# Performance work log

Hardware: AMD Instinct MI355X
Metric: run time of the kernel (lower is better)

The kernel has to match this reference:

```python
import jax, jax.numpy as jnp
import numpy as np

N = 100000          # nodes
E = 1600000         # edges (avg degree 16)
NUM_NODES = 100000  # embedding vocab
EMB = 128
HID = 64
G = 256             # graphs in the batch


def setup_inputs() -> dict:
    key = jax.random.key(0)
    ks = jax.random.split(key, 14)
    x_ids = jax.random.randint(ks[0], (N,), 0, NUM_NODES)
    edge_index = jax.random.randint(ks[1], (2, E), 0, N)
    batch = jnp.sort(jax.random.randint(ks[2], (N,), 0, G))
    s = 0.05
    emb = jax.random.normal(ks[3], (NUM_NODES, EMB), jnp.float32) * s
    W1 = jax.random.normal(ks[4], (EMB, HID), jnp.float32) * s
    b1 = jnp.zeros((HID,), jnp.float32)
    W2 = jax.random.normal(ks[5], (HID, HID), jnp.float32) * s
    b2 = jnp.zeros((HID,), jnp.float32)
    W3 = jax.random.normal(ks[6], (HID, HID), jnp.float32) * s
    b3 = jnp.zeros((HID,), jnp.float32)
    Wf1 = jax.random.normal(ks[7], (HID, HID), jnp.float32) * s
    bf1 = jnp.zeros((HID,), jnp.float32)
    Wf2 = jax.random.normal(ks[8], (HID, 1), jnp.float32) * s
    bf2 = jnp.zeros((1,), jnp.float32)
    return dict(x_ids=x_ids, edge_index=edge_index, batch=batch, emb=emb,
                W1=W1, b1=b1, W2=W2, b2=b2, W3=W3, b3=b3,
                Wf1=Wf1, bf1=bf1, Wf2=Wf2, bf2=bf2)


def gcn_conv(x, W, b, src, dst, num_nodes):
    # PyG GCNConv: x' = D^{-1/2} (A + I) D^{-1/2} (x W) + b
    xw = x @ W  # [N, out]
    ones = jnp.ones(src.shape[0], x.dtype)
    deg = jax.ops.segment_sum(ones, dst, num_segments=num_nodes) + 1.0  # self-loop
    dinv = jax.lax.rsqrt(deg)
    coef = dinv[src] * dinv[dst]  # per-edge norm
    agg = jax.ops.segment_sum(xw[src] * coef[:, None], dst, num_segments=num_nodes)
    agg = agg + xw * (dinv * dinv)[:, None]  # self-loop message
    return agg + b


def reference(x_ids, edge_index, batch, emb, W1, b1, W2, b2, W3, b3, Wf1, bf1, Wf2, bf2):
    src, dst = edge_index[0], edge_index[1]
    x = emb[x_ids]                                   # [N, EMB]
    x = jax.nn.relu(gcn_conv(x, W1, b1, src, dst, N))
    x = jax.nn.relu(gcn_conv(x, W2, b2, src, dst, N))
    x = jax.nn.relu(gcn_conv(x, W3, b3, src, dst, N))
    # global mean pool per graph
    counts = jax.ops.segment_sum(jnp.ones(N, x.dtype), batch, num_segments=G)
    pooled = jax.ops.segment_sum(x, batch, num_segments=G) / jnp.maximum(counts, 1.0)[:, None]
    h = jax.nn.relu(pooled @ Wf1 + bf1)
    out = (h @ Wf2 + bf2).squeeze(-1)                # [G]
    return jax.nn.sigmoid(out)
```

## Files before the change

kernel.cpp:

```cpp
#include <hip/hip_runtime.h>
#include <hip/hip_bf16.h>
#include <hip/hip_fp8.h>


typedef unsigned char u8;
typedef unsigned short u16;
typedef unsigned int u32;

#define FSCALE 256.0f
#define DINV_SCALE 0.0625f

__device__ __forceinline__ float fp8d(u32 b) {
#if __has_builtin(__builtin_amdgcn_cvt_f32_fp8)
  return __builtin_amdgcn_cvt_f32_fp8((int)b, 0);
#else
  __hip_fp8_e4m3 t; t.__x = (__hip_fp8_storage_t)b; return (float)t;
#endif
}
__device__ __forceinline__ u32 fp8e1(float f) {
#if __has_builtin(__builtin_amdgcn_cvt_pk_fp8_f32)
  return (u32)__builtin_amdgcn_cvt_pk_fp8_f32(f, 0.f, 0, false) & 0xffu;
#else
  __hip_fp8_e4m3 t(f); return (u32)t.__x;
#endif
}
__device__ __forceinline__ u32 fp8e4(float f0, float f1, float f2, float f3) {
#if __has_builtin(__builtin_amdgcn_cvt_pk_fp8_f32)
  int r = 0;
  r = __builtin_amdgcn_cvt_pk_fp8_f32(f0, f1, r, false);
  r = __builtin_amdgcn_cvt_pk_fp8_f32(f2, f3, r, true);
  return (u32)r;
#else
  __hip_fp8_e4m3 a(f0), b(f1), c(f2), d(f3);
  return (u32)a.__x | ((u32)b.__x << 8) | ((u32)c.__x << 16) | ((u32)d.__x << 24);
#endif
}

__global__ __launch_bounds__(256) void k_init(int* __restrict__ cnt8, int n8,
                                              u8* __restrict__ rowA, u8* __restrict__ rowB) {
  int i = blockIdx.x * blockDim.x + threadIdx.x;
  int stride = gridDim.x * blockDim.x;
  for (; i < n8; i += stride) cnt8[i] = 0;
  if (blockIdx.x == 0 && threadIdx.x < 64) {
    rowA[threadIdx.x] = 0;
    rowB[threadIdx.x] = 0;
  }
}

__global__ __launch_bounds__(256) void k_count_rank(const int* __restrict__ dst, int* __restrict__ cnt8,
                                                    int* __restrict__ rank, int e_count, int n) {
  int e = blockIdx.x * blockDim.x + threadIdx.x;
  if (e < e_count) {
    int p = blockIdx.x & 7;
    rank[e] = atomicAdd(&cnt8[p * n + dst[e]], 1);
  }
}

__global__ __launch_bounds__(256) void k_scan1(const int* __restrict__ cnt8, int n, int* __restrict__ bsum) {
  __shared__ int s[256];
  int b = blockIdx.x, t = threadIdx.x;
  int base = b * 1024;
  int sum = 0;
  #pragma unroll
  for (int i = 0; i < 4; ++i) {
    int idx = base + t + i * 256;
    if (idx < n) {
      int c = 0;
      #pragma unroll
      for (int q = 0; q < 8; ++q) c += cnt8[q * n + idx];
      sum += (c + 7) & ~7;
    }
  }
  s[t] = sum; __syncthreads();
  for (int off = 128; off > 0; off >>= 1) {
    if (t < off) s[t] += s[t + off];
    __syncthreads();
  }
  if (t == 0) bsum[b] = s[0];
}

__global__ __launch_bounds__(128) void k_scan2(int* __restrict__ bsum, int nb, int* __restrict__ total_out) {
  __shared__ int sh[128];
  int t = threadIdx.x;
  sh[t] = (t < nb) ? bsum[t] : 0;
  __syncthreads();
  for (int off = 1; off < 128; off <<= 1) {
    int x = sh[t];
    int y = (t >= off) ? sh[t - off] : 0;
    __syncthreads();
    sh[t] = x + y;
    __syncthreads();
  }
  if (t < nb) bsum[t] = (t == 0) ? 0 : sh[t - 1];
  if (t == 0) *total_out = sh[127];
}

__global__ __launch_bounds__(256) void k_scan3(int* __restrict__ cnt8, int n,
                                               const int* __restrict__ bsum_ex, int* __restrict__ offsets,
                                               float* __restrict__ dinv, u32* __restrict__ csr) {
  __shared__ int sh[256];
  int b = blockIdx.x, t = threadIdx.x;
  int base = b * 1024 + t * 4;
  int cq[4][8];
  int c[4], v[4];
  #pragma unroll
  for (int i = 0; i < 4; ++i) {
    c[i] = 0;
    #pragma unroll
    for (int q = 0; q < 8; ++q) {
      int x = (base + i < n) ? cnt8[q * n + base + i] : 0;
      cq[i][q] = x;
      c[i] += x;
    }
    v[i] = (c[i] + 7) & ~7;
    if (base + i < n) dinv[base + i] = rsqrtf((float)c[i] + 1.0f) * DINV_SCALE;
  }
  sh[t] = v[0] + v[1] + v[2] + v[3];
  __syncthreads();
  for (int off = 1; off < 256; off <<= 1) {
    int x = sh[t];
    int y = (t >= off) ? sh[t - off] : 0;
    __syncthreads();
    sh[t] = x + y;
    __syncthreads();
  }
  int run = bsum_ex[b] + ((t == 0) ? 0 : sh[t - 1]);
  #pragma unroll
  for (int i = 0; i < 4; ++i) {
    if (base + i < n) {
      offsets[base + i] = run;
      int pb = run;
      #pragma unroll
      for (int q = 0; q < 8; ++q) {
        cnt8[q * n + base + i] = pb;
        pb += cq[i][q];
      }
      for (int j = run + c[i]; j < run + v[i]; ++j) csr[j] = (u32)n;
      run += v[i];
    }
  }
  if (b == 0 && t == 0) dinv[n] = 0.f;
}

__global__ __launch_bounds__(256, 4) void k_mm1_scatter(
    const int* __restrict__ ids, const float* __restrict__ emb,
    const float* __restrict__ W1, u8* __restrict__ out, int n, int mmb,
    const int* __restrict__ src, const int* __restrict__ dst,
    const int* __restrict__ rank, const int* __restrict__ pbase,
    u32* __restrict__ csr, int e_count) {
  if ((int)blockIdx.x >= mmb) {
    int eb = blockIdx.x - mmb;
    int e = eb * 256 + threadIdx.x;
    if (e < e_count) {
      int p = eb & 7;
      int d = dst[e];
      int pos = pbase[p * n + d] + rank[e];
      __builtin_nontemporal_store((u32)src[e], &csr[pos]);
    }
    return;
  }

  const int lane = threadIdx.x & 63;
  const int w = threadIdx.x >> 6;
  const int r = blockIdx.x * 256 + w * 64 + lane;
  const int rid = ids[(r < n) ? r : (n - 1)];
  const float4* __restrict__ xrow = reinterpret_cast<const float4*>(emb + (size_t)rid * 128);

  float acc[64];
  #pragma unroll
  for (int j = 0; j < 64; ++j) acc[j] = 0.f;

  #pragma unroll 1
  for (int s = 0; s < 4; ++s) {
    float4 xb[8];
    #pragma unroll
    for (int i = 0; i < 8; ++i) xb[i] = xrow[s * 8 + i];
    const float* __restrict__ wbase = W1 + (size_t)(s * 32) * 64;
    #pragma unroll
    for (int i = 0; i < 8; ++i) {
      const float* __restrict__ w0 = wbase + (i * 4) * 64;
      #pragma unroll
      for (int j = 0; j < 64; ++j) {
        acc[j] = fmaf(xb[i].x, w0[j], acc[j]);
        acc[j] = fmaf(xb[i].y, w0[64 + j], acc[j]);
        acc[j] = fmaf(xb[i].z, w0[128 + j], acc[j]);
        acc[j] = fmaf(xb[i].w, w0[192 + j], acc[j]);
      }
    }
  }

  if (r < n) {
    u8* op = out + (size_t)r * 64;
    #pragma unroll
    for (int q = 0; q < 4; ++q) {
      uint4 pk;
      pk.x = fp8e4(acc[q * 16 + 0] * FSCALE, acc[q * 16 + 1] * FSCALE,
                   acc[q * 16 + 2] * FSCALE, acc[q * 16 + 3] * FSCALE);
      pk.y = fp8e4(acc[q * 16 + 4] * FSCALE, acc[q * 16 + 5] * FSCALE,
                   acc[q * 16 + 6] * FSCALE, acc[q * 16 + 7] * FSCALE);
      pk.z = fp8e4(acc[q * 16 + 8] * FSCALE, acc[q * 16 + 9] * FSCALE,
                   acc[q * 16 + 10] * FSCALE, acc[q * 16 + 11] * FSCALE);
      pk.w = fp8e4(acc[q * 16 + 12] * FSCALE, acc[q * 16 + 13] * FSCALE,
                   acc[q * 16 + 14] * FSCALE, acc[q * 16 + 15] * FSCALE);
      *reinterpret_cast<uint4*>(op + q * 16) = pk;
    }
  }
}


template <bool FINAL>
__global__ __launch_bounds__(256) void k_agg(const u8* __restrict__ xw, const u32* __restrict__ csr,
                                             const int* __restrict__ offs, const float* __restrict__ dinv,
                                             const float* __restrict__ bias, const float* __restrict__ Wn,
                                             u8* __restrict__ out, int n) {
  const int lane = threadIdx.x & 63;
  const int w = threadIdx.x >> 6;
  const float bl = bias[lane];
  const int ngroups = (n + 3) >> 2;
  const int nwaves = gridDim.x * 4;

  for (int grp = blockIdx.x * 4 + w; grp < ngroups; grp += nwaves) {
    const int v0 = grp * 4;
    const int c1 = (v0 + 1 < n) ? v0 + 1 : n;
    const int c2 = (v0 + 2 < n) ? v0 + 2 : n;
    const int c3 = (v0 + 3 < n) ? v0 + 3 : n;
    const int b0 = offs[v0], b1 = offs[c1], b2 = offs[c2], b3 = offs[c3];
    const int b4 = offs[(v0 + 4 < n) ? v0 + 4 : n];

    const float d0 = dinv[v0];
    const float d1 = dinv[(c1 < n) ? c1 : v0];
    const float d2 = dinv[(c2 < n) ? c2 : v0];
    const float d3 = dinv[(c3 < n) ? c3 : v0];
    float acc0 = fmaf(fp8d(xw[(size_t)v0 * 64 + lane]) * d0, d0, bl);
    float acc1 = (c1 < n) ? fmaf(fp8d(xw[(size_t)c1 * 64 + lane]) * d1, d1, bl) : 0.f;
    float acc2 = (c2 < n) ? fmaf(fp8d(xw[(size_t)c2 * 64 + lane]) * d2, d2, bl) : 0.f;
    float acc3 = (c3 < n) ? fmaf(fp8d(xw[(size_t)c3 * 64 + lane]) * d3, d3, bl) : 0.f;

    int e = b0;
    while (e < b4) {
      int cc = b4 - e;
      cc = (cc < 64) ? cc : 64;
      u32 ce = (u32)n;
      if (lane < cc) ce = csr[e + lane];
      for (int bs = 0; bs < cc; bs += 8) {
        float xv[8], dv[8];
        #pragma unroll
        for (int t = 0; t < 8; ++t) {
          int sb = __builtin_amdgcn_readlane((int)ce, bs + t);
          xv[t] = fp8d(xw[(size_t)sb * 64 + lane]);
          dv[t] = dinv[sb];
        }
        float tmp = 0.f;
        #pragma unroll
        for (int t = 0; t < 8; ++t) tmp = fmaf(xv[t], dv[t], tmp);
        const int ep = e + bs;
        if (ep < b1) acc0 = fmaf(tmp, d0, acc0);
        else if (ep < b2) acc1 = fmaf(tmp, d1, acc1);
        else if (ep < b3) acc2 = fmaf(tmp, d2, acc2);
        else acc3 = fmaf(tmp, d3, acc3);
      }
      e += cc;
    }

    float h0 = fmaxf(acc0, 0.f), h1 = fmaxf(acc1, 0.f);
    float h2 = fmaxf(acc2, 0.f), h3 = fmaxf(acc3, 0.f);
    if constexpr (FINAL) {
      out[(size_t)v0 * 64 + lane] = (u8)fp8e1(h0 * FSCALE);
      if (c1 < n) out[(size_t)c1 * 64 + lane] = (u8)fp8e1(h1 * FSCALE);
      if (c2 < n) out[(size_t)c2 * 64 + lane] = (u8)fp8e1(h2 * FSCALE);
      if (c3 < n) out[(size_t)c3 * 64 + lane] = (u8)fp8e1(h3 * FSCALE);
    } else {
      const int hb0 = __float_as_int(h0), hb1 = __float_as_int(h1);
      const int hb2 = __float_as_int(h2), hb3 = __float_as_int(h3);
      float o0 = 0.f, o1 = 0.f, o2 = 0.f, o3 = 0.f;
      #pragma unroll
      for (int k = 0; k < 64; ++k) {
        float wk = Wn[k * 64 + lane];
        o0 = fmaf(__int_as_float(__builtin_amdgcn_readlane(hb0, k)), wk, o0);
        o1 = fmaf(__int_as_float(__builtin_amdgcn_readlane(hb1, k)), wk, o1);
        o2 = fmaf(__int_as_float(__builtin_amdgcn_readlane(hb2, k)), wk, o2);
        o3 = fmaf(__int_as_float(__builtin_amdgcn_readlane(hb3, k)), wk, o3);
      }
      out[(size_t)v0 * 64 + lane] = (u8)fp8e1(o0 * FSCALE);
      if (c1 < n) out[(size_t)c1 * 64 + lane] = (u8)fp8e1(o1 * FSCALE);
      if (c2 < n) out[(size_t)c2 * 64 + lane] = (u8)fp8e1(o2 * FSCALE);
      if (c3 < n) out[(size_t)c3 * 64 + lane] = (u8)fp8e1(o3 * FSCALE);
    }
  }
}

__global__ __launch_bounds__(256) void k_pool(const u8* __restrict__ x, const int* __restrict__ batch, int n,
                                              const float* __restrict__ Wf1, const float* __restrict__ bf1,
                                              const float* __restrict__ Wf2, const float* __restrict__ bf2,
                                              float* __restrict__ out) {
  int g = blockIdx.x;
  int tid = threadIdx.x, lane = tid & 63, w = tid >> 6;
  int a = 0, b = n;
  while (a < b) { int m = (a + b) >> 1; if (batch[m] < g) a = m + 1; else b = m; }
  int lo = a;
  b = n;
  while (a < b) { int m = (a + b) >> 1; if (batch[m] < g + 1) a = m + 1; else b = m; }
  int hi = a;

  float acc = 0.f;
  for (int r = lo + w; r < hi; r += 4) acc += fp8d(x[(size_t)r * 64 + lane]);
  __shared__ float red[4][64];
  __shared__ float mean[64];
  red[w][lane] = acc;
  __syncthreads();
  if (w == 0) {
    float s = red[0][lane] + red[1][lane] + red[2][lane] + red[3][lane];
    mean[lane] = s / (fmaxf((float)(hi - lo), 1.0f) * FSCALE);
  }
  __syncthreads();
  if (w == 0) {
    float h = bf1[lane];
    #pragma unroll
    for (int k = 0; k < 64; ++k) h = fmaf(mean[k], Wf1[k * 64 + lane], h);
    h = fmaxf(h, 0.f);
    float vv = h * Wf2[lane];
    for (int off = 32; off > 0; off >>= 1) vv += __shfl_down(vv, off, 64);
    if (lane == 0) out[g] = 1.0f / (1.0f + expf(-(vv + bf2[0])));
  }
}

static inline char* align256(char* p) {
  return (char*)(((uintptr_t)p + 255) & ~(uintptr_t)255);
}

extern "C" void kernel_launch(void* const* d_in, const int* in_sizes, int n_in,
                              void* d_out, int out_size, void* d_ws, size_t ws_size,
                              hipStream_t stream) {
  const int*   x_ids = (const int*)d_in[0];
  const int*   edge  = (const int*)d_in[1];
  const int*   batch = (const int*)d_in[2];
  const float* emb   = (const float*)d_in[3];
  const float* W1    = (const float*)d_in[4];
  const float* b1    = (const float*)d_in[5];
  const float* W2    = (const float*)d_in[6];
  const float* b2    = (const float*)d_in[7];
  const float* W3    = (const float*)d_in[8];
  const float* b3    = (const float*)d_in[9];
  const float* Wf1   = (const float*)d_in[10];
  const float* bf1   = (const float*)d_in[11];
  const float* Wf2   = (const float*)d_in[12];
  const float* bf2   = (const float*)d_in[13];
  float* out = (float*)d_out;

  const int N = in_sizes[0];
  const int E = in_sizes[1] / 2;
  const int G = out_size;
  const int* e_src = edge;
  const int* e_dst = edge + E;

  const size_t EPAD = (size_t)E + 8 * (size_t)(N + 1) + 64;

  char* p = (char*)d_ws;
  u8*    bufA = (u8*)p;               p = align256(p + (size_t)(N + 1) * 64);
  u8*    bufB = (u8*)p;               p = align256(p + (size_t)(N + 1) * 64);
  u32*   csr  = (u32*)p;              p = align256(p + EPAD * 4);
  int*   rank = (int*)p;              p = align256(p + (size_t)E * 4);
  float* dinv = (float*)p;            p = align256(p + (size_t)(N + 1) * 4);
  int*   cnt8 = (int*)p;              p = align256(p + (size_t)8 * N * 4);
  int*   offs = (int*)p;              p = align256(p + (size_t)(N + 1) * 4);
  int*   bsum = (int*)p;              p = align256(p + (size_t)1024 * 4);
  (void)ws_size; (void)n_in;

  const int nb_scan = (N + 1023) / 1024;
  dim3 blk(256);

  k_init<<<dim3(512), blk, 0, stream>>>(cnt8, 8 * N, bufA + (size_t)N * 64, bufB + (size_t)N * 64);
  k_count_rank<<<dim3((E + 255) / 256), blk, 0, stream>>>(e_dst, cnt8, rank, E, N);
  k_scan1<<<dim3(nb_scan), blk, 0, stream>>>(cnt8, N, bsum);
  k_scan2<<<dim3(1), dim3(128), 0, stream>>>(bsum, nb_scan, offs + N);
  k_scan3<<<dim3(nb_scan), blk, 0, stream>>>(cnt8, N, bsum, offs, dinv, csr);

  const int mmb = (N + 255) / 256;
  const int scb = (E + 255) / 256;
  k_mm1_scatter<<<dim3(mmb + scb), blk, 0, stream>>>(
      x_ids, emb, W1, bufA, N, mmb,
      e_src, e_dst, rank, cnt8, csr, E);

  k_agg<false><<<dim3(2048), blk, 0, stream>>>(bufA, csr, offs, dinv, b1, W2, bufB, N);
  k_agg<false><<<dim3(2048), blk, 0, stream>>>(bufB, csr, offs, dinv, b2, W3, bufA, N);
  k_agg<true><<<dim3(2048), blk, 0, stream>>>(bufA, csr, offs, dinv, b3, nullptr, bufB, N);

  k_pool<<<dim3(G), blk, 0, stream>>>(bufB, batch, N, Wf1, bf1, Wf2, bf2, out);
}
```

Baseline: 397.9 us.

## Pre-scale node features by source dinv and pipeline fixed 64-edge gathers

Stored fp8 node features are now pre-multiplied by their own inverse-sqrt degree. This happens in the first matmul epilogue and in each aggregation's output, so the edge loop no longer gathers dinv[src] per edge and just sums decoded values. The inner loop now always processes a full 64-edge chunk with two 8-register gather buffers interleaved with compute, to overlap loads and arithmetic. Out-of-range lanes read the zero padding row, and the CSR pad grows to cover over-reads. The fixed chunk size wastes gathers on short tails, and folding dinv into the stored values changes the fp8 quantization range.

```diff
diff --git a/kernel.cpp b/kernel.cpp
--- a/kernel.cpp
+++ b/kernel.cpp
@@ -8,7 +8,8 @@
 typedef unsigned int u32;
 
 #define FSCALE 256.0f
-#define DINV_SCALE 0.0625f
+#define SINV (1.0f / 256.0f)
+#define S2 65536.0f
 
 __device__ __forceinline__ float fp8d(u32 b) {
 #if __has_builtin(__builtin_amdgcn_cvt_f32_fp8)
@@ -97,7 +98,7 @@
 
 __global__ __launch_bounds__(256) void k_scan3(int* __restrict__ cnt8, int n,
                                                const int* __restrict__ bsum_ex, int* __restrict__ offsets,
-                                               float* __restrict__ dinv, u32* __restrict__ csr) {
+                                               float* __restrict__ dsc, u32* __restrict__ csr) {
   __shared__ int sh[256];
   int b = blockIdx.x, t = threadIdx.x;
   int base = b * 1024 + t * 4;
@@ -113,7 +114,7 @@
       c[i] += x;
     }
     v[i] = (c[i] + 7) & ~7;
-    if (base + i < n) dinv[base + i] = rsqrtf((float)c[i] + 1.0f) * DINV_SCALE;
+    if (base + i < n) dsc[base + i] = rsqrtf((float)c[i] + 1.0f) * SINV;
   }
   sh[t] = v[0] + v[1] + v[2] + v[3];
   __syncthreads();
@@ -139,7 +140,7 @@
       run += v[i];
     }
   }
-  if (b == 0 && t == 0) dinv[n] = 0.f;
+  if (b == 0 && t == 0) dsc[n] = 0.f;
 }
 
 __global__ __launch_bounds__(256, 4) void k_mm1_scatter(
@@ -147,7 +148,7 @@
     const float* __restrict__ W1, u8* __restrict__ out, int n, int mmb,
     const int* __restrict__ src, const int* __restrict__ dst,
     const int* __restrict__ rank, const int* __restrict__ pbase,
-    u32* __restrict__ csr, int e_count) {
+    const float* __restrict__ dsc, u32* __restrict__ csr, int e_count) {
   if ((int)blockIdx.x >= mmb) {
     int eb = blockIdx.x - mmb;
     int e = eb * 256 + threadIdx.x;
@@ -163,7 +164,9 @@
   const int lane = threadIdx.x & 63;
   const int w = threadIdx.x >> 6;
   const int r = blockIdx.x * 256 + w * 64 + lane;
-  const int rid = ids[(r < n) ? r : (n - 1)];
+  const int rc = (r < n) ? r : (n - 1);
+  const int rid = ids[rc];
+  const float zs = dsc[rc] * S2;
   const float4* __restrict__ xrow = reinterpret_cast<const float4*>(emb + (size_t)rid * 128);
 
   float acc[64];
@@ -194,23 +197,42 @@
     #pragma unroll
     for (int q = 0; q < 4; ++q) {
       uint4 pk;
-      pk.x = fp8e4(acc[q * 16 + 0] * FSCALE, acc[q * 16 + 1] * FSCALE,
-                   acc[q * 16 + 2] * FSCALE, acc[q * 16 + 3] * FSCALE);
-      pk.y = fp8e4(acc[q * 16 + 4] * FSCALE, acc[q * 16 + 5] * FSCALE,
-                   acc[q * 16 + 6] * FSCALE, acc[q * 16 + 7] * FSCALE);
-      pk.z = fp8e4(acc[q * 16 + 8] * FSCALE, acc[q * 16 + 9] * FSCALE,
-                   acc[q * 16 + 10] * FSCALE, acc[q * 16 + 11] * FSCALE);
-      pk.w = fp8e4(acc[q * 16 + 12] * FSCALE, acc[q * 16 + 13] * FSCALE,
-                   acc[q * 16 + 14] * FSCALE, acc[q * 16 + 15] * FSCALE);
+      pk.x = fp8e4(acc[q * 16 + 0] * zs, acc[q * 16 + 1] * zs,
+                   acc[q * 16 + 2] * zs, acc[q * 16 + 3] * zs);
+      pk.y = fp8e4(acc[q * 16 + 4] * zs, acc[q * 16 + 5] * zs,
+                   acc[q * 16 + 6] * zs, acc[q * 16 + 7] * zs);
+      pk.z = fp8e4(acc[q * 16 + 8] * zs, acc[q * 16 + 9] * zs,
+                   acc[q * 16 + 10] * zs, acc[q * 16 + 11] * zs);
+      pk.w = fp8e4(acc[q * 16 + 12] * zs, acc[q * 16 + 13] * zs,
+                   acc[q * 16 + 14] * zs, acc[q * 16 + 15] * zs);
       *reinterpret_cast<uint4*>(op + q * 16) = pk;
     }
   }
 }
 
 
+#define G8(dstreg, OFF)                                                      \
+  _Pragma("unroll")                                                          \
+  for (int t_ = 0; t_ < 8; ++t_) {                                           \
+    int sb_ = __builtin_amdgcn_readlane((int)ce, (OFF) + t_);                \
+    dstreg[t_] = (u32)z[(size_t)sb_ * 64 + lane];                            \
+  }
+
+#define C8(srcreg, OFF)                                                      \
+  {                                                                          \
+    float tmp_ = 0.f;                                                        \
+    _Pragma("unroll")                                                        \
+    for (int t_ = 0; t_ < 8; ++t_) tmp_ += fp8d(srcreg[t_]);                 \
+    const int ep_ = e + (OFF);                                               \
+    if (ep_ < b1) acc0 = fmaf(tmp_, d0, acc0);                               \
+    else if (ep_ < b2) acc1 = fmaf(tmp_, d1, acc1);                          \
+    else if (ep_ < b3) acc2 = fmaf(tmp_, d2, acc2);                          \
+    else acc3 = fmaf(tmp_, d3, acc3);                                        \
+  }
+
 template <bool FINAL>
-__global__ __launch_bounds__(256) void k_agg(const u8* __restrict__ xw, const u32* __restrict__ csr,
-                                             const int* __restrict__ offs, const float* __restrict__ dinv,
+__global__ __launch_bounds__(256) void k_agg(const u8* __restrict__ z, const u32* __restrict__ csr,
+                                             const int* __restrict__ offs, const float* __restrict__ dsc,
                                              const float* __restrict__ bias, const float* __restrict__ Wn,
                                              u8* __restrict__ out, int n) {
   const int lane = threadIdx.x & 63;
@@ -227,39 +249,37 @@
     const int b0 = offs[v0], b1 = offs[c1], b2 = offs[c2], b3 = offs[c3];
     const int b4 = offs[(v0 + 4 < n) ? v0 + 4 : n];
 
-    const float d0 = dinv[v0];
-    const float d1 = dinv[(c1 < n) ? c1 : v0];
-    const float d2 = dinv[(c2 < n) ? c2 : v0];
-    const float d3 = dinv[(c3 < n) ? c3 : v0];
-    float acc0 = fmaf(fp8d(xw[(size_t)v0 * 64 + lane]) * d0, d0, bl);
-    float acc1 = (c1 < n) ? fmaf(fp8d(xw[(size_t)c1 * 64 + lane]) * d1, d1, bl) : 0.f;
-    float acc2 = (c2 < n) ? fmaf(fp8d(xw[(size_t)c2 * 64 + lane]) * d2, d2, bl) : 0.f;
-    float acc3 = (c3 < n) ? fmaf(fp8d(xw[(size_t)c3 * 64 + lane]) * d3, d3, bl) : 0.f;
+    const float d0 = dsc[v0];
+    const float d1 = dsc[(c1 < n) ? c1 : v0];
+    const float d2 = dsc[(c2 < n) ? c2 : v0];
+    const float d3 = dsc[(c3 < n) ? c3 : v0];
+    float acc0 = fmaf(fp8d(z[(size_t)v0 * 64 + lane]), d0, bl);
+    float acc1 = (c1 < n) ? fmaf(fp8d(z[(size_t)c1 * 64 + lane]), d1, bl) : 0.f;
+    float acc2 = (c2 < n) ? fmaf(fp8d(z[(size_t)c2 * 64 + lane]), d2, bl) : 0.f;
+    float acc3 = (c3 < n) ? fmaf(fp8d(z[(size_t)c3 * 64 + lane]), d3, bl) : 0.f;
 
     int e = b0;
     while (e < b4) {
-      int cc = b4 - e;
-      cc = (cc < 64) ? cc : 64;
       u32 ce = (u32)n;
-      if (lane < cc) ce = csr[e + lane];
-      for (int bs = 0; bs < cc; bs += 8) {
-        float xv[8], dv[8];
-        #pragma unroll
-        for (int t = 0; t < 8; ++t) {
-          int sb = __builtin_amdgcn_readlane((int)ce, bs + t);
-          xv[t] = fp8d(xw[(size_t)sb * 64 + lane]);
-          dv[t] = dinv[sb];
-        }
-        float tmp = 0.f;
-        #pragma unroll
-        for (int t = 0; t < 8; ++t) tmp = fmaf(xv[t], dv[t], tmp);
-        const int ep = e + bs;
-        if (ep < b1) acc0 = fmaf(tmp, d0, acc0);
-        else if (ep < b2) acc1 = fmaf(tmp, d1, acc1);
-        else if (ep < b3) acc2 = fmaf(tmp, d2, acc2);
-        else acc3 = fmaf(tmp, d3, acc3);
-      }
-      e += cc;
+      if (lane < b4 - e) ce = csr[e + lane];
+      u32 gA[8], gB[8];
+      G8(gA, 0)
+      G8(gB, 8)
+      C8(gA, 0)
+      G8(gA, 16)
+      C8(gB, 8)
+      G8(gB, 24)
+      C8(gA, 16)
+      G8(gA, 32)
+      C8(gB, 24)
+      G8(gB, 40)
+      C8(gA, 32)
+      G8(gA, 48)
+      C8(gB, 40)
+      G8(gB, 56)
+      C8(gA, 48)
+      C8(gB, 56)
+      e += 64;
     }
 
     float h0 = fmaxf(acc0, 0.f), h1 = fmaxf(acc1, 0.f);
@@ -281,10 +301,10 @@
         o2 = fmaf(__int_as_float(__builtin_amdgcn_readlane(hb2, k)), wk, o2);
         o3 = fmaf(__int_as_float(__builtin_amdgcn_readlane(hb3, k)), wk, o3);
       }
-      out[(size_t)v0 * 64 + lane] = (u8)fp8e1(o0 * FSCALE);
-      if (c1 < n) out[(size_t)c1 * 64 + lane] = (u8)fp8e1(o1 * FSCALE);
-      if (c2 < n) out[(size_t)c2 * 64 + lane] = (u8)fp8e1(o2 * FSCALE);
-      if (c3 < n) out[(size_t)c3 * 64 + lane] = (u8)fp8e1(o3 * FSCALE);
+      out[(size_t)v0 * 64 + lane] = (u8)fp8e1(o0 * d0 * S2);
+      if (c1 < n) out[(size_t)c1 * 64 + lane] = (u8)fp8e1(o1 * d1 * S2);
+      if (c2 < n) out[(size_t)c2 * 64 + lane] = (u8)fp8e1(o2 * d2 * S2);
+      if (c3 < n) out[(size_t)c3 * 64 + lane] = (u8)fp8e1(o3 * d3 * S2);
     }
   }
 }
@@ -353,14 +373,14 @@
   const int* e_src = edge;
   const int* e_dst = edge + E;
 
-  const size_t EPAD = (size_t)E + 8 * (size_t)(N + 1) + 64;
+  const size_t EPAD = (size_t)E + 8 * (size_t)(N + 1) + 128;
 
   char* p = (char*)d_ws;
   u8*    bufA = (u8*)p;               p = align256(p + (size_t)(N + 1) * 64);
   u8*    bufB = (u8*)p;               p = align256(p + (size_t)(N + 1) * 64);
   u32*   csr  = (u32*)p;              p = align256(p + EPAD * 4);
   int*   rank = (int*)p;              p = align256(p + (size_t)E * 4);
-  float* dinv = (float*)p;            p = align256(p + (size_t)(N + 1) * 4);
+  float* dsc  = (float*)p;            p = align256(p + (size_t)(N + 1) * 4);
   int*   cnt8 = (int*)p;              p = align256(p + (size_t)8 * N * 4);
   int*   offs = (int*)p;              p = align256(p + (size_t)(N + 1) * 4);
   int*   bsum = (int*)p;              p = align256(p + (size_t)1024 * 4);
@@ -373,17 +393,17 @@
   k_count_rank<<<dim3((E + 255) / 256), blk, 0, stream>>>(e_dst, cnt8, rank, E, N);
   k_scan1<<<dim3(nb_scan), blk, 0, stream>>>(cnt8, N, bsum);
   k_scan2<<<dim3(1), dim3(128), 0, stream>>>(bsum, nb_scan, offs + N);
-  k_scan3<<<dim3(nb_scan), blk, 0, stream>>>(cnt8, N, bsum, offs, dinv, csr);
+  k_scan3<<<dim3(nb_scan), blk, 0, stream>>>(cnt8, N, bsum, offs, dsc, csr);
 
   const int mmb = (N + 255) / 256;
   const int scb = (E + 255) / 256;
   k_mm1_scatter<<<dim3(mmb + scb), blk, 0, stream>>>(
       x_ids, emb, W1, bufA, N, mmb,
-      e_src, e_dst, rank, cnt8, csr, E);
-
-  k_agg<false><<<dim3(2048), blk, 0, stream>>>(bufA, csr, offs, dinv, b1, W2, bufB, N);
-  k_agg<false><<<dim3(2048), blk, 0, stream>>>(bufB, csr, offs, dinv, b2, W3, bufA, N);
-  k_agg<true><<<dim3(2048), blk, 0, stream>>>(bufA, csr, offs, dinv, b3, nullptr, bufB, N);
+      e_src, e_dst, rank, cnt8, dsc, csr, E);
+
+  k_agg<false><<<dim3(2048), blk, 0, stream>>>(bufA, csr, offs, dsc, b1, W2, bufB, N);
+  k_agg<false><<<dim3(2048), blk, 0, stream>>>(bufB, csr, offs, dsc, b2, W3, bufA, N);
+  k_agg<true><<<dim3(2048), blk, 0, stream>>>(bufA, csr, offs, dsc, b3, nullptr, bufB, N);
 
   k_pool<<<dim3(G), blk, 0, stream>>>(bufB, batch, N, Wf1, bf1, Wf2, bf2, out);
 }
```

Result: faster. 386.0 us (-3.0%).
